# Performance work log

Measured on AMD Instinct MI355X. Metric: run time of the kernel, lower is better.

The kernel has to match this reference:

```python
import jax, jax.numpy as jnp
import numpy as np

N = 50000
E = 800000
IN_DIM = 128
HID = 64
OUT_DIM = 128
NEG_SLOPE = 0.2  # PyG GATConv default


def _add_self_loops(src, dst, edge_attr, n):
    # PyG GATConv(add_self_loops=True) with edge_dim uses fill_value='mean':
    # self-loop edge_attr = mean of edge_attr of incoming edges per node.
    deg = jax.ops.segment_sum(jnp.ones((src.shape[0],), edge_attr.dtype), dst, num_segments=n)
    loop_attr = jax.ops.segment_sum(edge_attr, dst, num_segments=n) / jnp.maximum(deg, 1.0)[:, None]
    loop = jnp.arange(n, dtype=src.dtype)
    return (jnp.concatenate([src, loop]), jnp.concatenate([dst, loop]),
            jnp.concatenate([edge_attr, loop_attr], axis=0))


def _gat_conv(x, src, dst, edge_attr, W, We, a_src, a_dst, a_edge, bias, heads, out_dim, concat, n):
    src, dst, edge_attr = _add_self_loops(src, dst, edge_attr, n)
    h = (x @ W).reshape(n, heads, out_dim)                      # [N,H,D]
    he = (edge_attr @ We).reshape(-1, heads, out_dim)           # [E',H,D]
    alpha_src = jnp.einsum('nhd,hd->nh', h, a_src)
    alpha_dst = jnp.einsum('nhd,hd->nh', h, a_dst)
    alpha_edge = jnp.einsum('ehd,hd->eh', he, a_edge)
    alpha = jax.nn.leaky_relu(alpha_src[src] + alpha_dst[dst] + alpha_edge, NEG_SLOPE)  # [E',H]
    # segment softmax over edges grouped by destination node
    amax = jax.ops.segment_max(alpha, dst, num_segments=n)
    amax = jnp.where(jnp.isfinite(amax), amax, 0.0)
    ex = jnp.exp(alpha - amax[dst])
    denom = jax.ops.segment_sum(ex, dst, num_segments=n)
    coef = ex / (denom[dst] + 1e-16)                            # [E',H]
    msg = h[src] * coef[:, :, None]                             # [E',H,D]
    out = jax.ops.segment_sum(msg, dst, num_segments=n)         # [N,H,D]
    out = out.reshape(n, heads * out_dim) if concat else out.mean(axis=1)
    return out + bias


def setup_inputs() -> dict:
    key = jax.random.key(0)
    ks = jax.random.split(key, 16)
    s = 0.05
    inp = {
        'x': jax.random.normal(ks[0], (N, IN_DIM), jnp.float32),
        'edge_index': jax.random.randint(ks[1], (2, E), 0, N, dtype=jnp.int64),
        'edge_attr': jax.random.normal(ks[2], (E, 2), jnp.float32),
        # gat1: heads=4, concat -> out 4*HID
        'W1': jax.random.normal(ks[3], (IN_DIM, 4 * HID), jnp.float32) * s,
        'We1': jax.random.normal(ks[4], (2, 4 * HID), jnp.float32) * s,
        'asrc1': jax.random.normal(ks[5], (4, HID), jnp.float32) * s,
        'adst1': jax.random.normal(ks[6], (4, HID), jnp.float32) * s,
        'aedge1': jax.random.normal(ks[7], (4, HID), jnp.float32) * s,
        'b1': jnp.zeros((4 * HID,), jnp.float32),
        # gat2: heads=1, concat=False -> out OUT_DIM
        'W2': jax.random.normal(ks[8], (4 * HID, OUT_DIM), jnp.float32) * s,
        'We2': jax.random.normal(ks[9], (2, OUT_DIM), jnp.float32) * s,
        'asrc2': jax.random.normal(ks[10], (1, OUT_DIM), jnp.float32) * s,
        'adst2': jax.random.normal(ks[11], (1, OUT_DIM), jnp.float32) * s,
        'aedge2': jax.random.normal(ks[12], (1, OUT_DIM), jnp.float32) * s,
        'b2': jnp.zeros((OUT_DIM,), jnp.float32),
    }
    return inp


def reference(x, edge_index, edge_attr, W1, We1, asrc1, adst1, aedge1, b1,
              W2, We2, asrc2, adst2, aedge2, b2):
    src, dst = edge_index[0], edge_index[1]
    # dropout layers are identity in eval mode
    h = _gat_conv(x, src, dst, edge_attr, W1, We1, asrc1, adst1, aedge1, b1,
                  heads=4, out_dim=HID, concat=True, n=x.shape[0])
    h = jax.nn.elu(h)
    out = _gat_conv(h, src, dst, edge_attr, W2, We2, asrc2, adst2, aedge2, b2,
                    heads=1, out_dim=OUT_DIM, concat=False, n=x.shape[0])
    return out
```

## Files before the change

### kernel.cpp

```cpp
#include <hip/hip_runtime.h>
#include <hip/hip_bf16.h>

#define NN 50000
#define EE 800000
#define SCAN_B 2048
#define NB ((NN + SCAN_B - 1) / SCAN_B)


typedef short bf16x8 __attribute__((ext_vector_type(8)));
typedef float f32x4  __attribute__((ext_vector_type(4)));

__device__ __forceinline__ float bf2f(unsigned short u) {
    return __uint_as_float(((unsigned)u) << 16);
}
__device__ __forceinline__ unsigned short f2bf(float f) {
    unsigned b = __float_as_uint(f);
    b += 0x7fffu + ((b >> 16) & 1u);
    return (unsigned short)(b >> 16);
}
__device__ __forceinline__ float2 bfpair(unsigned u) {
    return make_float2(__uint_as_float(u << 16), __uint_as_float(u & 0xffff0000u));
}

__global__ void k_prep(const float* __restrict__ We1, const float* __restrict__ ae1,
                       const float* __restrict__ We2, const float* __restrict__ ae2,
                       float* __restrict__ v,
                       const float* __restrict__ W1, unsigned short* __restrict__ W1t,
                       const float* __restrict__ W2, unsigned short* __restrict__ W2t,
                       const int* __restrict__ ei, int* __restrict__ idg,
                       int* __restrict__ rank,
                       const float* __restrict__ x, unsigned short* __restrict__ xb) {
    int bid = blockIdx.x, t = threadIdx.x;
    if (bid == 0) {
        if (t < 8) {
            int c = t >> 2, h = t & 3;
            float s = 0.f;
            for (int d = 0; d < 64; d++) s += We1[c * 256 + h * 64 + d] * ae1[h * 64 + d];
            v[c * 4 + h] = s;
        } else if (t < 10) {
            int c = t - 8;
            float s = 0.f;
            for (int d = 0; d < 128; d++) s += We2[c * 128 + d] * ae2[d];
            v[8 + c] = s;
        }
    } else if (bid <= 256) {
        int idx = (bid - 1) * 256 + t;
        if (idx < 32768) {
            int k = idx >> 8, n = idx & 255;
            W1t[n * 128 + k] = f2bf(W1[idx]);
        } else {
            int i = idx - 32768;
            int k = i >> 7, n = i & 127;
            W2t[n * 256 + k] = f2bf(W2[i]);
        }
    } else if (bid <= 256 + 3125) {
        int e = (bid - 257) * 256 + t;
        if (e < EE) rank[e] = atomicAdd(&idg[ei[EE + e]], 1);
    } else {
        int i = (bid - 3382) * 256 + t;
        if (i < NN * 128 / 4) {
            float4 vv = ((const float4*)x)[i];
            ushort4 o;
            o.x = f2bf(vv.x); o.y = f2bf(vv.y); o.z = f2bf(vv.z); o.w = f2bf(vv.w);
            ((ushort4*)xb)[i] = o;
        }
    }
}

__global__ void k_scan1(const int* __restrict__ idg, int* __restrict__ rowptr,
                        int* __restrict__ bsum) {
    __shared__ int sh[512];
    int t = threadIdx.x;
    int base = blockIdx.x * SCAN_B + t * 4;
    int v[4]; int s = 0;
    #pragma unroll
    for (int j = 0; j < 4; j++) {
        int i = base + j;
        v[j] = (i < NN) ? idg[i] : 0;
        s += v[j];
    }
    sh[t] = s;
    __syncthreads();
    for (int off = 1; off < 512; off <<= 1) {
        int a = (t >= off) ? sh[t - off] : 0;
        __syncthreads();
        sh[t] += a;
        __syncthreads();
    }
    int run = sh[t] - s;
    #pragma unroll
    for (int j = 0; j < 4; j++) {
        int i = base + j;
        if (i < NN) rowptr[i] = run;
        run += v[j];
    }
    if (t == 511) bsum[blockIdx.x] = sh[511];
}

__global__ void k_scan2(const int* __restrict__ bsum, int* __restrict__ boff,
                        int* __restrict__ rowptr) {
    if (threadIdx.x == 0) {
        int acc = 0;
        for (int b = 0; b < NB; b++) { boff[b] = acc; acc += bsum[b]; }
        rowptr[NN] = acc;
    }
}

__global__ void k_scan3(int* __restrict__ rowptr, const int* __restrict__ boff) {
    int t = threadIdx.x;
    int i = blockIdx.x * SCAN_B + t * 4;
    int off = boff[blockIdx.x];
    #pragma unroll
    for (int j = 0; j < 4; j++)
        if (i + j < NN) rowptr[i + j] += off;
}

__global__ void k_scatter(const int* __restrict__ ei, const float* __restrict__ eattr,
                          const int* __restrict__ rowptr, const int* __restrict__ rank,
                          int2* __restrict__ slot) {
    int e = blockIdx.x * blockDim.x + threadIdx.x;
    if (e >= EE) return;
    int s = ei[e], d = ei[EE + e];
    int p = rowptr[d] + rank[e];
    float2 a = ((const float2*)eattr)[e];
    unsigned a0 = f2bf(a.x), a1 = f2bf(a.y);
    slot[p] = make_int2(s, (int)(a0 | (a1 << 16)));
}

template <int K, int NT, int H>
__global__ __launch_bounds__(256) void gemm_mfma(const unsigned short* __restrict__ A,
                                                 const unsigned short* __restrict__ Bt,
                                                 unsigned short* __restrict__ C,
                                                 const float* __restrict__ avs,
                                                 const float* __restrict__ avd,
                                                 float* __restrict__ asrc,
                                                 float* __restrict__ adst,
                                                 int M, int N) {
    int wave = threadIdx.x >> 6, lane = threadIdx.x & 63;
    int l16 = lane & 15, quad = lane >> 4;
    int m0 = blockIdx.y * 128 + wave * 32;
    int n0 = blockIdx.x * (NT * 16);

    f32x4 acc[2][NT];
    #pragma unroll
    for (int mt = 0; mt < 2; mt++)
        #pragma unroll
        for (int nt = 0; nt < NT; nt++)
            acc[mt][nt] = (f32x4){0.f, 0.f, 0.f, 0.f};

    int ar0 = min(m0 + l16, M - 1);
    int ar1 = min(m0 + 16 + l16, M - 1);
    const unsigned short* a0 = A + (size_t)ar0 * K + quad * 8;
    const unsigned short* a1 = A + (size_t)ar1 * K + quad * 8;
    const unsigned short* bp = Bt + (size_t)(n0 + l16) * K + quad * 8;

    #pragma unroll
    for (int k0 = 0; k0 < K; k0 += 32) {
        bf16x8 af0 = *(const bf16x8*)(a0 + k0);
        bf16x8 af1 = *(const bf16x8*)(a1 + k0);
        #pragma unroll
        for (int nt = 0; nt < NT; nt++) {
            bf16x8 bf = *(const bf16x8*)(bp + (size_t)nt * 16 * K + k0);
            acc[0][nt] = __builtin_amdgcn_mfma_f32_16x16x32_bf16(af0, bf, acc[0][nt], 0, 0, 0);
            acc[1][nt] = __builtin_amdgcn_mfma_f32_16x16x32_bf16(af1, bf, acc[1][nt], 0, 0, 0);
        }
    }

    #pragma unroll
    for (int mt = 0; mt < 2; mt++)
        #pragma unroll
        for (int reg = 0; reg < 4; reg++) {
            int row = m0 + mt * 16 + quad * 4 + reg;
            if (row < M) {
                #pragma unroll
                for (int nt = 0; nt < NT; nt++)
                    C[(size_t)row * N + n0 + nt * 16 + l16] = f2bf(acc[mt][nt][reg]);
            }
        }

    float ws[NT], wd[NT];
    #pragma unroll
    for (int nt = 0; nt < NT; nt++) {
        ws[nt] = avs[n0 + nt * 16 + l16];
        wd[nt] = avd[n0 + nt * 16 + l16];
    }
    int hh = n0 >> 6;
    #pragma unroll
    for (int mt = 0; mt < 2; mt++)
        #pragma unroll
        for (int reg = 0; reg < 4; reg++) {
            int row = m0 + mt * 16 + quad * 4 + reg;
            float s1 = 0.f, s2 = 0.f;
            #pragma unroll
            for (int nt = 0; nt < NT; nt++) {
                float c = acc[mt][nt][reg];
                s1 += c * ws[nt];
                s2 += c * wd[nt];
            }
            #pragma unroll
            for (int off = 1; off < 16; off <<= 1) {
                s1 += __shfl_xor(s1, off);
                s2 += __shfl_xor(s2, off);
            }
            if (l16 == 0 && row < M) {
                asrc[row * H + hh] = s1;
                adst[row * H + hh] = s2;
            }
        }
}

__global__ __launch_bounds__(256) void k_agg1(const int* __restrict__ rowptr,
                       const int2* __restrict__ slot, const float* __restrict__ asrc,
                       const float* __restrict__ adst, const float* __restrict__ v,
                       const unsigned short* __restrict__ hb, const float* __restrict__ b1,
                       unsigned short* __restrict__ h2b) {
    int node = blockIdx.x * 4 + (threadIdx.x >> 6);
    if (node >= NN) return;
    int lane = threadIdx.x & 63;
    int h2 = lane >> 5;
    int hl = lane & 31;
    int hd = hl >> 3;
    int beg = rowptr[node], end = rowptr[node + 1];
    float pd = adst[node * 4 + hd];
    float vh0 = v[hd], vh1 = v[4 + hd];
    float acc[8] = {};
    float den = 0.f, s0 = 0.f, s1 = 0.f;
    const unsigned short* hbq = hb + hl * 8;

    int cnt = end - beg;
    int safeLast = max(end - 1, 0);
    int mend = beg + (cnt & ~1);

    int2 sl0 = slot[min(beg + h2, safeLast)];
    int2 sl1 = slot[min(beg + 2 + h2, safeLast)];

    auto body = [&](int2 cur) {
        int s = cur.x;
        float2 a = bfpair((unsigned)cur.y);
        float al = asrc[s * 4 + hd] + pd + a.x * vh0 + a.y * vh1;
        al = (al > 0.f) ? al : 0.2f * al;
        float e = __expf(al);
        s0 += a.x; s1 += a.y; den += e;
        uint4 r = *(const uint4*)(hbq + (size_t)s * 256);
        float2 p;
        p = bfpair(r.x); acc[0] += e * p.x; acc[1] += e * p.y;
        p = bfpair(r.y); acc[2] += e * p.x; acc[3] += e * p.y;
        p = bfpair(r.z); acc[4] += e * p.x; acc[5] += e * p.y;
        p = bfpair(r.w); acc[6] += e * p.x; acc[7] += e * p.y;
    };

    #pragma unroll 2
    for (int pb = beg; pb < mend; pb += 2) {
        int2 cur = sl0;
        sl0 = sl1;
        sl1 = slot[min(pb + 4 + h2, safeLast)];
        body(cur);
    }
    if (h2 == 0 && mend < end) body(sl0);

    #pragma unroll
    for (int k = 0; k < 8; k++) acc[k] += __shfl_down(acc[k], 32);
    den += __shfl_xor(den, 32);
    s0  += __shfl_xor(s0, 32);
    s1  += __shfl_xor(s1, 32);

    float dg = fmaxf((float)cnt, 1.0f);
    float als = asrc[node * 4 + hd] + pd + (s0 / dg) * vh0 + (s1 / dg) * vh1;
    als = (als > 0.f) ? als : 0.2f * als;
    float exs = __expf(als);
    den += exs;

    if (h2 == 0) {
        uint4 r = *(const uint4*)(hbq + (size_t)node * 256);
        float2 p;
        p = bfpair(r.x); acc[0] += exs * p.x; acc[1] += exs * p.y;
        p = bfpair(r.y); acc[2] += exs * p.x; acc[3] += exs * p.y;
        p = bfpair(r.z); acc[4] += exs * p.x; acc[5] += exs * p.y;
        p = bfpair(r.w); acc[6] += exs * p.x; acc[7] += exs * p.y;
        float inv = 1.f / (den + 1e-16f);
        short ov[8];
        #pragma unroll
        for (int k = 0; k < 8; k++) {
            float va = acc[k] * inv + b1[hl * 8 + k];
            va = (va > 0.f) ? va : __expf(va) - 1.f;
            ov[k] = (short)f2bf(va);
        }
        bf16x8 o8 = {ov[0], ov[1], ov[2], ov[3], ov[4], ov[5], ov[6], ov[7]};
        *(bf16x8*)(h2b + (size_t)node * 256 + hl * 8) = o8;
    }
}

__global__ __launch_bounds__(256) void k_agg2(const int* __restrict__ rowptr,
                       const int2* __restrict__ slot, const float* __restrict__ asrc,
                       const float* __restrict__ adst, const float* __restrict__ v,
                       const unsigned short* __restrict__ gb, const float* __restrict__ b2,
                       float* __restrict__ outp) {
    int node = blockIdx.x * 4 + (threadIdx.x >> 6);
    if (node >= NN) return;
    int lane = threadIdx.x & 63;
    int q  = lane >> 4;
    int ql = lane & 15;
    int beg = rowptr[node], end = rowptr[node + 1];
    float ad = adst[node];
    float v0 = v[0], v1 = v[1];
    float acc[8] = {};
    float den = 0.f, s0 = 0.f, s1 = 0.f;
    const unsigned short* gbq = gb + ql * 8;

    int cnt = end - beg;
    int safeLast = max(end - 1, 0);
    int mend = beg + (cnt & ~3);

    int2 sl0 = slot[min(beg + q, safeLast)];
    int2 sl1 = slot[min(beg + 4 + q, safeLast)];

    auto body = [&](int2 cur) {
        int s = cur.x;
        float2 a = bfpair((unsigned)cur.y);
        float al = asrc[s] + ad + a.x * v0 + a.y * v1;
        al = (al > 0.f) ? al : 0.2f * al;
        float e = __expf(al);
        s0 += a.x; s1 += a.y; den += e;
        uint4 r = *(const uint4*)(gbq + (size_t)s * 128);
        float2 p;
        p = bfpair(r.x); acc[0] += e * p.x; acc[1] += e * p.y;
        p = bfpair(r.y); acc[2] += e * p.x; acc[3] += e * p.y;
        p = bfpair(r.z); acc[4] += e * p.x; acc[5] += e * p.y;
        p = bfpair(r.w); acc[6] += e * p.x; acc[7] += e * p.y;
    };

    #pragma unroll 2
    for (int pb = beg; pb < mend; pb += 4) {
        int2 cur = sl0;
        sl0 = sl1;
        sl1 = slot[min(pb + 8 + q, safeLast)];
        body(cur);
    }
    if (mend + q < end) body(sl0);

    #pragma unroll
    for (int k = 0; k < 8; k++) {
        acc[k] += __shfl_down(acc[k], 32);
        acc[k] += __shfl_down(acc[k], 16);
    }
    den += __shfl_xor(den, 16); den += __shfl_xor(den, 32);
    s0  += __shfl_xor(s0, 16);  s0  += __shfl_xor(s0, 32);
    s1  += __shfl_xor(s1, 16);  s1  += __shfl_xor(s1, 32);

    float dg = fmaxf((float)cnt, 1.0f);
    float als = asrc[node] + ad + (s0 / dg) * v0 + (s1 / dg) * v1;
    als = (als > 0.f) ? als : 0.2f * als;
    float exs = __expf(als);
    den += exs;

    if (q == 0) {
        uint4 r = *(const uint4*)(gbq + (size_t)node * 128);
        float2 p;
        p = bfpair(r.x); acc[0] += exs * p.x; acc[1] += exs * p.y;
        p = bfpair(r.y); acc[2] += exs * p.x; acc[3] += exs * p.y;
        p = bfpair(r.z); acc[4] += exs * p.x; acc[5] += exs * p.y;
        p = bfpair(r.w); acc[6] += exs * p.x; acc[7] += exs * p.y;
        float inv = 1.f / (den + 1e-16f);
        float4 o0, o1;
        o0.x = acc[0] * inv + b2[ql * 8 + 0];
        o0.y = acc[1] * inv + b2[ql * 8 + 1];
        o0.z = acc[2] * inv + b2[ql * 8 + 2];
        o0.w = acc[3] * inv + b2[ql * 8 + 3];
        o1.x = acc[4] * inv + b2[ql * 8 + 4];
        o1.y = acc[5] * inv + b2[ql * 8 + 5];
        o1.z = acc[6] * inv + b2[ql * 8 + 6];
        o1.w = acc[7] * inv + b2[ql * 8 + 7];
        *(float4*)(outp + (size_t)node * 128 + ql * 8)     = o0;
        *(float4*)(outp + (size_t)node * 128 + ql * 8 + 4) = o1;
    }
}

extern "C" void kernel_launch(void* const* d_in, const int* in_sizes, int n_in,
                              void* d_out, int out_size, void* d_ws, size_t ws_size,
                              hipStream_t stream) {
    const float* x     = (const float*)d_in[0];
    const int*   ei    = (const int*)d_in[1];
    const float* eattr = (const float*)d_in[2];
    const float* W1    = (const float*)d_in[3];
    const float* We1   = (const float*)d_in[4];
    const float* as1   = (const float*)d_in[5];
    const float* ad1   = (const float*)d_in[6];
    const float* ae1   = (const float*)d_in[7];
    const float* b1    = (const float*)d_in[8];
    const float* W2    = (const float*)d_in[9];
    const float* We2   = (const float*)d_in[10];
    const float* as2   = (const float*)d_in[11];
    const float* ad2   = (const float*)d_in[12];
    const float* ae2   = (const float*)d_in[13];
    const float* b2    = (const float*)d_in[14];
    float* out = (float*)d_out;

    int* idg    = (int*)d_ws;
    int* rank   = idg + NN;
    int* rowptr = rank + EE;
    int* bsum   = rowptr + NN + 16;
    int* boff   = bsum + 32;
    int2* slot  = (int2*)(boff + 32);
    float* asrc1 = (float*)(slot + EE);
    float* adst1 = asrc1 + 4 * NN;
    float* asrc2 = adst1 + 4 * NN;
    float* adst2 = asrc2 + NN;
    float* vbuf  = adst2 + NN;
    unsigned short* ub = (unsigned short*)(((uintptr_t)(vbuf + 64) + 63) & ~(uintptr_t)63);
    unsigned short* x_bf  = ub;
    unsigned short* W1t   = x_bf + (size_t)NN * 128;
    unsigned short* W2t   = W1t + 32768;
    unsigned short* h1_bf = W2t + 32768;
    unsigned short* h2_bf = h1_bf + (size_t)NN * 256;
    unsigned short* g2_bf = h2_bf + (size_t)NN * 256;

    hipMemsetAsync(idg, 0, (size_t)NN * sizeof(int), stream);

    k_prep<<<9632, 256, 0, stream>>>(We1, ae1, We2, ae2, vbuf, W1, W1t, W2, W2t,
                                     ei, idg, rank, x, x_bf);
    k_scan1<<<NB, 512, 0, stream>>>(idg, rowptr, bsum);
    k_scan2<<<1, 64, 0, stream>>>(bsum, boff, rowptr);
    k_scan3<<<NB, 512, 0, stream>>>(rowptr, boff);
    k_scatter<<<(EE + 255) / 256, 256, 0, stream>>>(ei, eattr, rowptr, rank, slot);

    gemm_mfma<128, 4, 4><<<dim3(4, (NN + 127) / 128), 256, 0, stream>>>(
        x_bf, W1t, h1_bf, as1, ad1, asrc1, adst1, NN, 256);
    k_agg1<<<(NN + 3) / 4, 256, 0, stream>>>(rowptr, slot, asrc1, adst1, vbuf,
                                             h1_bf, b1, h2_bf);

    gemm_mfma<256, 8, 1><<<dim3(1, (NN + 127) / 128), 256, 0, stream>>>(
        h2_bf, W2t, g2_bf, as2, ad2, asrc2, adst2, NN, 128);
    k_agg2<<<(NN + 3) / 4, 256, 0, stream>>>(rowptr, slot, asrc2, adst2, vbuf + 8,
                                             g2_bf, b2, out);
}
```

Measured before the change: 327.7 us.

## Aggregate raw x before projecting in layer one, fold attention vectors into W1

Layer one now computes attention logits directly from x, using W1 folded with the source and destination attention vectors (Asd). It then aggregates the 128-wide bf16 x rows per head into a 512-wide per-node buffer, and only afterwards runs a per-head MFMA projection with bias and ELU. The gather in the edge loop touches 256 bytes per edge instead of 512, at the cost of four times as many accumulators per lane and a larger intermediate buffer written and read by the projection. The intermediate buffer is reused for the layer-two GEMM output.

```diff
diff --git a/kernel.cpp b/kernel.cpp
--- a/kernel.cpp
+++ b/kernel.cpp
@@ -25,6 +25,8 @@
 __global__ void k_prep(const float* __restrict__ We1, const float* __restrict__ ae1,
                        const float* __restrict__ We2, const float* __restrict__ ae2,
                        float* __restrict__ v,
+                       const float* __restrict__ as1, const float* __restrict__ ad1,
+                       float* __restrict__ Asd,
                        const float* __restrict__ W1, unsigned short* __restrict__ W1t,
                        const float* __restrict__ W2, unsigned short* __restrict__ W2t,
                        const int* __restrict__ ei, int* __restrict__ idg,
@@ -43,6 +45,15 @@
             for (int d = 0; d < 128; d++) s += We2[c * 128 + d] * ae2[d];
             v[8 + c] = s;
         }
+        #pragma unroll 1
+        for (int idx = t; idx < 1024; idx += 256) {
+            int k = idx >> 3, j = idx & 7;
+            const float* a = (j < 4) ? as1 : ad1;
+            int h = j & 3;
+            float s = 0.f;
+            for (int c = 0; c < 64; c++) s += W1[k * 256 + h * 64 + c] * a[h * 64 + c];
+            Asd[idx] = s;
+        }
     } else if (bid <= 256) {
         int idx = (bid - 1) * 256 + t;
         if (idx < 32768) {
@@ -125,6 +136,203 @@
     float2 a = ((const float2*)eattr)[e];
     unsigned a0 = f2bf(a.x), a1 = f2bf(a.y);
     slot[p] = make_int2(s, (int)(a0 | (a1 << 16)));
+}
+
+__global__ __launch_bounds__(256) void k_attn1(const unsigned short* __restrict__ xb,
+                       const float* __restrict__ Asd,
+                       float* __restrict__ asrc, float* __restrict__ adst) {
+    int node = blockIdx.x * 4 + (threadIdx.x >> 6);
+    if (node >= NN) return;
+    int lane = threadIdx.x & 63;
+    unsigned xw = *(const unsigned*)(xb + (size_t)node * 128 + lane * 2);
+    float2 xc = bfpair(xw);
+    const float4* A4 = (const float4*)Asd;
+    float4 s0 = A4[lane * 4 + 0];
+    float4 d0 = A4[lane * 4 + 1];
+    float4 s1 = A4[lane * 4 + 2];
+    float4 d1 = A4[lane * 4 + 3];
+    float r[8];
+    r[0] = xc.x * s0.x + xc.y * s1.x;
+    r[1] = xc.x * s0.y + xc.y * s1.y;
+    r[2] = xc.x * s0.z + xc.y * s1.z;
+    r[3] = xc.x * s0.w + xc.y * s1.w;
+    r[4] = xc.x * d0.x + xc.y * d1.x;
+    r[5] = xc.x * d0.y + xc.y * d1.y;
+    r[6] = xc.x * d0.z + xc.y * d1.z;
+    r[7] = xc.x * d0.w + xc.y * d1.w;
+    #pragma unroll
+    for (int off = 1; off < 64; off <<= 1)
+        #pragma unroll
+        for (int j = 0; j < 8; j++) r[j] += __shfl_xor(r[j], off);
+    if (lane == 0) {
+        *(float4*)(asrc + node * 4) = make_float4(r[0], r[1], r[2], r[3]);
+        *(float4*)(adst + node * 4) = make_float4(r[4], r[5], r[6], r[7]);
+    }
+}
+
+__global__ __launch_bounds__(256) void k_agg1x(const int* __restrict__ rowptr,
+                       const int2* __restrict__ slot, const float* __restrict__ asrc,
+                       const float* __restrict__ adst, const float* __restrict__ v,
+                       const unsigned short* __restrict__ xb,
+                       unsigned short* __restrict__ Sx) {
+    int node = blockIdx.x * 4 + (threadIdx.x >> 6);
+    if (node >= NN) return;
+    int lane = threadIdx.x & 63;
+    int q  = lane >> 4;
+    int ql = lane & 15;
+    int beg = rowptr[node], end = rowptr[node + 1];
+    float4 pd4 = *(const float4*)(adst + node * 4);
+    float pd[4] = {pd4.x, pd4.y, pd4.z, pd4.w};
+    float v0[4] = {v[0], v[1], v[2], v[3]};
+    float v1[4] = {v[4], v[5], v[6], v[7]};
+    float acc[4][8] = {};
+    float den[4] = {};
+    float s0 = 0.f, s1 = 0.f;
+    const unsigned short* xbq = xb + ql * 8;
+
+    int cnt = end - beg;
+    int safeLast = max(end - 1, 0);
+    int mend = beg + (cnt & ~3);
+
+    int2 sl0 = slot[min(beg + q, safeLast)];
+    int2 sl1 = slot[min(beg + 4 + q, safeLast)];
+
+    auto body = [&](int2 cur) {
+        int s = cur.x;
+        float2 a = bfpair((unsigned)cur.y);
+        float4 as4 = *(const float4*)(asrc + s * 4);
+        float as_[4] = {as4.x, as4.y, as4.z, as4.w};
+        uint4 r = *(const uint4*)(xbq + (size_t)s * 128);
+        float e[4];
+        #pragma unroll
+        for (int h = 0; h < 4; h++) {
+            float al = as_[h] + pd[h] + a.x * v0[h] + a.y * v1[h];
+            al = (al > 0.f) ? al : 0.2f * al;
+            e[h] = __expf(al);
+            den[h] += e[h];
+        }
+        s0 += a.x; s1 += a.y;
+        float xx[8];
+        float2 p;
+        p = bfpair(r.x); xx[0] = p.x; xx[1] = p.y;
+        p = bfpair(r.y); xx[2] = p.x; xx[3] = p.y;
+        p = bfpair(r.z); xx[4] = p.x; xx[5] = p.y;
+        p = bfpair(r.w); xx[6] = p.x; xx[7] = p.y;
+        #pragma unroll
+        for (int h = 0; h < 4; h++)
+            #pragma unroll
+            for (int c = 0; c < 8; c++) acc[h][c] += e[h] * xx[c];
+    };
+
+    #pragma unroll 2
+    for (int pb = beg; pb < mend; pb += 4) {
+        int2 cur = sl0;
+        sl0 = sl1;
+        sl1 = slot[min(pb + 8 + q, safeLast)];
+        body(cur);
+    }
+    if (mend + q < end) body(sl0);
+
+    #pragma unroll
+    for (int h = 0; h < 4; h++)
+        #pragma unroll
+        for (int c = 0; c < 8; c++) {
+            acc[h][c] += __shfl_down(acc[h][c], 32);
+            acc[h][c] += __shfl_down(acc[h][c], 16);
+        }
+    #pragma unroll
+    for (int h = 0; h < 4; h++) {
+        den[h] += __shfl_xor(den[h], 16);
+        den[h] += __shfl_xor(den[h], 32);
+    }
+    s0 += __shfl_xor(s0, 16); s0 += __shfl_xor(s0, 32);
+    s1 += __shfl_xor(s1, 16); s1 += __shfl_xor(s1, 32);
+
+    float dg = fmaxf((float)cnt, 1.0f);
+    float4 an4 = *(const float4*)(asrc + node * 4);
+    float an[4] = {an4.x, an4.y, an4.z, an4.w};
+    float exs[4];
+    #pragma unroll
+    for (int h = 0; h < 4; h++) {
+        float als = an[h] + pd[h] + (s0 / dg) * v0[h] + (s1 / dg) * v1[h];
+        als = (als > 0.f) ? als : 0.2f * als;
+        exs[h] = __expf(als);
+        den[h] += exs[h];
+    }
+
+    if (q == 0) {
+        uint4 r = *(const uint4*)(xbq + (size_t)node * 128);
+        float xx[8];
+        float2 p;
+        p = bfpair(r.x); xx[0] = p.x; xx[1] = p.y;
+        p = bfpair(r.y); xx[2] = p.x; xx[3] = p.y;
+        p = bfpair(r.z); xx[4] = p.x; xx[5] = p.y;
+        p = bfpair(r.w); xx[6] = p.x; xx[7] = p.y;
+        #pragma unroll
+        for (int h = 0; h < 4; h++) {
+            float inv = 1.f / (den[h] + 1e-16f);
+            short ov[8];
+            #pragma unroll
+            for (int c = 0; c < 8; c++)
+                ov[c] = (short)f2bf((acc[h][c] + exs[h] * xx[c]) * inv);
+            bf16x8 o8 = {ov[0], ov[1], ov[2], ov[3], ov[4], ov[5], ov[6], ov[7]};
+            *(bf16x8*)(Sx + (size_t)node * 512 + h * 128 + ql * 8) = o8;
+        }
+    }
+}
+
+__global__ __launch_bounds__(256) void k_proj1(const unsigned short* __restrict__ Sx,
+                       const unsigned short* __restrict__ W1t,
+                       const float* __restrict__ b1,
+                       unsigned short* __restrict__ h2b) {
+    int h = blockIdx.x;
+    int wave = threadIdx.x >> 6, lane = threadIdx.x & 63;
+    int l16 = lane & 15, quad = lane >> 4;
+    int m0 = blockIdx.y * 128 + wave * 32;
+
+    f32x4 acc[2][4];
+    #pragma unroll
+    for (int mt = 0; mt < 2; mt++)
+        #pragma unroll
+        for (int nt = 0; nt < 4; nt++)
+            acc[mt][nt] = (f32x4){0.f, 0.f, 0.f, 0.f};
+
+    int ar0 = min(m0 + l16, NN - 1);
+    int ar1 = min(m0 + 16 + l16, NN - 1);
+    const unsigned short* a0 = Sx + (size_t)ar0 * 512 + h * 128 + quad * 8;
+    const unsigned short* a1 = Sx + (size_t)ar1 * 512 + h * 128 + quad * 8;
+    const unsigned short* bp = W1t + (size_t)(h * 64 + l16) * 128 + quad * 8;
+
+    #pragma unroll
+    for (int k0 = 0; k0 < 128; k0 += 32) {
+        bf16x8 af0 = *(const bf16x8*)(a0 + k0);
+        bf16x8 af1 = *(const bf16x8*)(a1 + k0);
+        #pragma unroll
+        for (int nt = 0; nt < 4; nt++) {
+            bf16x8 bf = *(const bf16x8*)(bp + (size_t)nt * 16 * 128 + k0);
+            acc[0][nt] = __builtin_amdgcn_mfma_f32_16x16x32_bf16(af0, bf, acc[0][nt], 0, 0, 0);
+            acc[1][nt] = __builtin_amdgcn_mfma_f32_16x16x32_bf16(af1, bf, acc[1][nt], 0, 0, 0);
+        }
+    }
+
+    float bia[4];
+    #pragma unroll
+    for (int nt = 0; nt < 4; nt++) bia[nt] = b1[h * 64 + nt * 16 + l16];
+
+    #pragma unroll
+    for (int mt = 0; mt < 2; mt++)
+        #pragma unroll
+        for (int reg = 0; reg < 4; reg++) {
+            int row = m0 + mt * 16 + quad * 4 + reg;
+            if (row < NN) {
+                #pragma unroll
+                for (int nt = 0; nt < 4; nt++) {
+                    float va = acc[mt][nt][reg] + bia[nt];
+                    va = (va > 0.f) ? va : __expf(va) - 1.f;
+                    h2b[(size_t)row * 256 + h * 64 + nt * 16 + l16] = f2bf(va);
+                }
+            }
+        }
 }
 
 template <int K, int NT, int H>
@@ -207,87 +415,6 @@
                 adst[row * H + hh] = s2;
             }
         }
-}
-
-__global__ __launch_bounds__(256) void k_agg1(const int* __restrict__ rowptr,
-                       const int2* __restrict__ slot, const float* __restrict__ asrc,
-                       const float* __restrict__ adst, const float* __restrict__ v,
-                       const unsigned short* __restrict__ hb, const float* __restrict__ b1,
-                       unsigned short* __restrict__ h2b) {
-    int node = blockIdx.x * 4 + (threadIdx.x >> 6);
-    if (node >= NN) return;
-    int lane = threadIdx.x & 63;
-    int h2 = lane >> 5;
-    int hl = lane & 31;
-    int hd = hl >> 3;
-    int beg = rowptr[node], end = rowptr[node + 1];
-    float pd = adst[node * 4 + hd];
-    float vh0 = v[hd], vh1 = v[4 + hd];
-    float acc[8] = {};
-    float den = 0.f, s0 = 0.f, s1 = 0.f;
-    const unsigned short* hbq = hb + hl * 8;
-
-    int cnt = end - beg;
-    int safeLast = max(end - 1, 0);
-    int mend = beg + (cnt & ~1);
-
-    int2 sl0 = slot[min(beg + h2, safeLast)];
-    int2 sl1 = slot[min(beg + 2 + h2, safeLast)];
-
-    auto body = [&](int2 cur) {
-        int s = cur.x;
-        float2 a = bfpair((unsigned)cur.y);
-        float al = asrc[s * 4 + hd] + pd + a.x * vh0 + a.y * vh1;
-        al = (al > 0.f) ? al : 0.2f * al;
-        float e = __expf(al);
-        s0 += a.x; s1 += a.y; den += e;
-        uint4 r = *(const uint4*)(hbq + (size_t)s * 256);
-        float2 p;
-        p = bfpair(r.x); acc[0] += e * p.x; acc[1] += e * p.y;
-        p = bfpair(r.y); acc[2] += e * p.x; acc[3] += e * p.y;
-        p = bfpair(r.z); acc[4] += e * p.x; acc[5] += e * p.y;
-        p = bfpair(r.w); acc[6] += e * p.x; acc[7] += e * p.y;
-    };
-
-    #pragma unroll 2
-    for (int pb = beg; pb < mend; pb += 2) {
-        int2 cur = sl0;
-        sl0 = sl1;
-        sl1 = slot[min(pb + 4 + h2, safeLast)];
-        body(cur);
-    }
-    if (h2 == 0 && mend < end) body(sl0);
-
-    #pragma unroll
-    for (int k = 0; k < 8; k++) acc[k] += __shfl_down(acc[k], 32);
-    den += __shfl_xor(den, 32);
-    s0  += __shfl_xor(s0, 32);
-    s1  += __shfl_xor(s1, 32);
-
-    float dg = fmaxf((float)cnt, 1.0f);
-    float als = asrc[node * 4 + hd] + pd + (s0 / dg) * vh0 + (s1 / dg) * vh1;
-    als = (als > 0.f) ? als : 0.2f * als;
-    float exs = __expf(als);
-    den += exs;
-
-    if (h2 == 0) {
-        uint4 r = *(const uint4*)(hbq + (size_t)node * 256);
-        float2 p;
-        p = bfpair(r.x); acc[0] += exs * p.x; acc[1] += exs * p.y;
-        p = bfpair(r.y); acc[2] += exs * p.x; acc[3] += exs * p.y;
-        p = bfpair(r.z); acc[4] += exs * p.x; acc[5] += exs * p.y;
-        p = bfpair(r.w); acc[6] += exs * p.x; acc[7] += exs * p.y;
-        float inv = 1.f / (den + 1e-16f);
-        short ov[8];
-        #pragma unroll
-        for (int k = 0; k < 8; k++) {
-            float va = acc[k] * inv + b1[hl * 8 + k];
-            va = (va > 0.f) ? va : __expf(va) - 1.f;
-            ov[k] = (short)f2bf(va);
-        }
-        bf16x8 o8 = {ov[0], ov[1], ov[2], ov[3], ov[4], ov[5], ov[6], ov[7]};
-        *(bf16x8*)(h2b + (size_t)node * 256 + hl * 8) = o8;
-    }
 }
 
 __global__ __launch_bounds__(256) void k_agg2(const int* __restrict__ rowptr,
@@ -406,27 +533,28 @@
     float* asrc2 = adst1 + 4 * NN;
     float* adst2 = asrc2 + NN;
     float* vbuf  = adst2 + NN;
-    unsigned short* ub = (unsigned short*)(((uintptr_t)(vbuf + 64) + 63) & ~(uintptr_t)63);
+    float* Asd   = vbuf + 64;
+    unsigned short* ub = (unsigned short*)(((uintptr_t)(Asd + 1024) + 63) & ~(uintptr_t)63);
     unsigned short* x_bf  = ub;
     unsigned short* W1t   = x_bf + (size_t)NN * 128;
     unsigned short* W2t   = W1t + 32768;
-    unsigned short* h1_bf = W2t + 32768;
-    unsigned short* h2_bf = h1_bf + (size_t)NN * 256;
-    unsigned short* g2_bf = h2_bf + (size_t)NN * 256;
+    unsigned short* Sx    = W2t + 32768;
+    unsigned short* h2_bf = Sx + (size_t)NN * 512;
+    unsigned short* g2_bf = Sx;
 
     hipMemsetAsync(idg, 0, (size_t)NN * sizeof(int), stream);
 
-    k_prep<<<9632, 256, 0, stream>>>(We1, ae1, We2, ae2, vbuf, W1, W1t, W2, W2t,
-                                     ei, idg, rank, x, x_bf);
+    k_prep<<<9632, 256, 0, stream>>>(We1, ae1, We2, ae2, vbuf, as1, ad1, Asd,
+                                     W1, W1t, W2, W2t, ei, idg, rank, x, x_bf);
     k_scan1<<<NB, 512, 0, stream>>>(idg, rowptr, bsum);
     k_scan2<<<1, 64, 0, stream>>>(bsum, boff, rowptr);
     k_scan3<<<NB, 512, 0, stream>>>(rowptr, boff);
     k_scatter<<<(EE + 255) / 256, 256, 0, stream>>>(ei, eattr, rowptr, rank, slot);
 
-    gemm_mfma<128, 4, 4><<<dim3(4, (NN + 127) / 128), 256, 0, stream>>>(
-        x_bf, W1t, h1_bf, as1, ad1, asrc1, adst1, NN, 256);
-    k_agg1<<<(NN + 3) / 4, 256, 0, stream>>>(rowptr, slot, asrc1, adst1, vbuf,
-                                             h1_bf, b1, h2_bf);
+    k_attn1<<<(NN + 3) / 4, 256, 0, stream>>>(x_bf, Asd, asrc1, adst1);
+    k_agg1x<<<(NN + 3) / 4, 256, 0, stream>>>(rowptr, slot, asrc1, adst1, vbuf,
+                                              x_bf, Sx);
+    k_proj1<<<dim3(4, (NN + 127) / 128), 256, 0, stream>>>(Sx, W1t, b1, h2_bf);
 
     gemm_mfma<256, 8, 1><<<dim3(1, (NN + 127) / 128), 256, 0, stream>>>(
         h2_bf, W2t, g2_bf, as2, ad2, asrc2, adst2, NN, 128);
```

Result: slower. 353.2 us (+7.8%).

## Merge scan into one block, fuse scatter with GEMM1, use exp2

Applied to the files above, without the earlier changes.

Replaces the three-kernel prefix scan with a single 1024-thread block scan. Fuses the edge scatter into the first GEMM launch as extra blocks so both run concurrently, saving launches. Pre-scales the attention vectors by log2(e) so softmax exponentials use the hardware exp2 instruction directly. The single-block scan serializes 49 elements per thread, which may be slower per element but avoids two kernel launches.

```diff
diff --git a/kernel.cpp b/kernel.cpp
--- a/kernel.cpp
+++ b/kernel.cpp
@@ -3,16 +3,13 @@
 
 #define NN 50000
 #define EE 800000
-#define SCAN_B 2048
-#define NB ((NN + SCAN_B - 1) / SCAN_B)
+#define LOG2E 1.44269504088896340736f
+#define GB1 1564
 
 
 typedef short bf16x8 __attribute__((ext_vector_type(8)));
 typedef float f32x4  __attribute__((ext_vector_type(4)));
 
-__device__ __forceinline__ float bf2f(unsigned short u) {
-    return __uint_as_float(((unsigned)u) << 16);
-}
 __device__ __forceinline__ unsigned short f2bf(float f) {
     unsigned b = __float_as_uint(f);
     b += 0x7fffu + ((b >> 16) & 1u);
@@ -36,12 +33,12 @@
             int c = t >> 2, h = t & 3;
             float s = 0.f;
             for (int d = 0; d < 64; d++) s += We1[c * 256 + h * 64 + d] * ae1[h * 64 + d];
-            v[c * 4 + h] = s;
+            v[c * 4 + h] = s * LOG2E;
         } else if (t < 10) {
             int c = t - 8;
             float s = 0.f;
             for (int d = 0; d < 128; d++) s += We2[c * 128 + d] * ae2[d];
-            v[8 + c] = s;
+            v[8 + c] = s * LOG2E;
         }
     } else if (bid <= 256) {
         int idx = (bid - 1) * 256 + t;
@@ -67,79 +64,50 @@
     }
 }
 
-__global__ void k_scan1(const int* __restrict__ idg, int* __restrict__ rowptr,
-                        int* __restrict__ bsum) {
-    __shared__ int sh[512];
+__global__ __launch_bounds__(1024) void k_scanA(const int* __restrict__ idg,
+                                                int* __restrict__ rowptr) {
+    __shared__ int sh[1024];
     int t = threadIdx.x;
-    int base = blockIdx.x * SCAN_B + t * 4;
-    int v[4]; int s = 0;
-    #pragma unroll
-    for (int j = 0; j < 4; j++) {
+    int base = t * 49;
+    int s = 0;
+    for (int j = 0; j < 49; j++) {
         int i = base + j;
-        v[j] = (i < NN) ? idg[i] : 0;
-        s += v[j];
+        s += (i < NN) ? idg[i] : 0;
     }
     sh[t] = s;
     __syncthreads();
-    for (int off = 1; off < 512; off <<= 1) {
+    for (int off = 1; off < 1024; off <<= 1) {
         int a = (t >= off) ? sh[t - off] : 0;
         __syncthreads();
         sh[t] += a;
         __syncthreads();
     }
     int run = sh[t] - s;
-    #pragma unroll
-    for (int j = 0; j < 4; j++) {
+    for (int j = 0; j < 49; j++) {
         int i = base + j;
-        if (i < NN) rowptr[i] = run;
-        run += v[j];
-    }
-    if (t == 511) bsum[blockIdx.x] = sh[511];
-}
-
-__global__ void k_scan2(const int* __restrict__ bsum, int* __restrict__ boff,
-                        int* __restrict__ rowptr) {
-    if (threadIdx.x == 0) {
-        int acc = 0;
-        for (int b = 0; b < NB; b++) { boff[b] = acc; acc += bsum[b]; }
-        rowptr[NN] = acc;
-    }
-}
-
-__global__ void k_scan3(int* __restrict__ rowptr, const int* __restrict__ boff) {
-    int t = threadIdx.x;
-    int i = blockIdx.x * SCAN_B + t * 4;
-    int off = boff[blockIdx.x];
-    #pragma unroll
-    for (int j = 0; j < 4; j++)
-        if (i + j < NN) rowptr[i + j] += off;
-}
-
-__global__ void k_scatter(const int* __restrict__ ei, const float* __restrict__ eattr,
-                          const int* __restrict__ rowptr, const int* __restrict__ rank,
-                          int2* __restrict__ slot) {
-    int e = blockIdx.x * blockDim.x + threadIdx.x;
-    if (e >= EE) return;
-    int s = ei[e], d = ei[EE + e];
-    int p = rowptr[d] + rank[e];
-    float2 a = ((const float2*)eattr)[e];
-    unsigned a0 = f2bf(a.x), a1 = f2bf(a.y);
-    slot[p] = make_int2(s, (int)(a0 | (a1 << 16)));
+        if (i < NN) {
+            int val = idg[i];
+            rowptr[i] = run;
+            run += val;
+        }
+    }
+    if (t == 1023) rowptr[NN] = sh[1023];
 }
 
 template <int K, int NT, int H>
-__global__ __launch_bounds__(256) void gemm_mfma(const unsigned short* __restrict__ A,
-                                                 const unsigned short* __restrict__ Bt,
-                                                 unsigned short* __restrict__ C,
-                                                 const float* __restrict__ avs,
-                                                 const float* __restrict__ avd,
-                                                 float* __restrict__ asrc,
-                                                 float* __restrict__ adst,
-                                                 int M, int N) {
+__device__ __forceinline__ void gemm_body(int bx, int by,
+                                          const unsigned short* __restrict__ A,
+                                          const unsigned short* __restrict__ Bt,
+                                          unsigned short* __restrict__ C,
+                                          const float* __restrict__ avs,
+                                          const float* __restrict__ avd,
+                                          float* __restrict__ asrc,
+                                          float* __restrict__ adst,
+                                          int M, int N) {
     int wave = threadIdx.x >> 6, lane = threadIdx.x & 63;
     int l16 = lane & 15, quad = lane >> 4;
-    int m0 = blockIdx.y * 128 + wave * 32;
-    int n0 = blockIdx.x * (NT * 16);
+    int m0 = by * 128 + wave * 32;
+    int n0 = bx * (NT * 16);
 
     f32x4 acc[2][NT];
     #pragma unroll
@@ -181,8 +149,8 @@
     float ws[NT], wd[NT];
     #pragma unroll
     for (int nt = 0; nt < NT; nt++) {
-        ws[nt] = avs[n0 + nt * 16 + l16];
-        wd[nt] = avd[n0 + nt * 16 + l16];
+        ws[nt] = avs[n0 + nt * 16 + l16] * LOG2E;
+        wd[nt] = avd[n0 + nt * 16 + l16] * LOG2E;
     }
     int hh = n0 >> 6;
     #pragma unroll
@@ -209,6 +177,37 @@
         }
 }
 
+__global__ __launch_bounds__(256) void k_sg(const unsigned short* __restrict__ xb,
+                       const unsigned short* __restrict__ W1t,
+                       unsigned short* __restrict__ h1b,
+                       const float* __restrict__ as1, const float* __restrict__ ad1,
+                       float* __restrict__ asrc1, float* __restrict__ adst1,
+                       const int* __restrict__ ei, const float* __restrict__ eattr,
+                       const int* __restrict__ rowptr, const int* __restrict__ rank,
+                       int2* __restrict__ slot) {
+    int bid = blockIdx.x;
+    if (bid < GB1) {
+        gemm_body<128, 4, 4>(bid & 3, bid >> 2, xb, W1t, h1b, as1, ad1,
+                             asrc1, adst1, NN, 256);
+    } else {
+        int e = (bid - GB1) * 256 + threadIdx.x;
+        if (e >= EE) return;
+        int s = ei[e], d = ei[EE + e];
+        int p = rowptr[d] + rank[e];
+        float2 a = ((const float2*)eattr)[e];
+        unsigned a0 = f2bf(a.x), a1 = f2bf(a.y);
+        slot[p] = make_int2(s, (int)(a0 | (a1 << 16)));
+    }
+}
+
+__global__ __launch_bounds__(256) void k_gemm2(const unsigned short* __restrict__ A,
+                       const unsigned short* __restrict__ Bt,
+                       unsigned short* __restrict__ C,
+                       const float* __restrict__ avs, const float* __restrict__ avd,
+                       float* __restrict__ asrc, float* __restrict__ adst) {
+    gemm_body<256, 8, 1>(0, blockIdx.x, A, Bt, C, avs, avd, asrc, adst, NN, 128);
+}
+
 __global__ __launch_bounds__(256) void k_agg1(const int* __restrict__ rowptr,
                        const int2* __restrict__ slot, const float* __restrict__ asrc,
                        const float* __restrict__ adst, const float* __restrict__ v,
@@ -239,7 +238,7 @@
         float2 a = bfpair((unsigned)cur.y);
         float al = asrc[s * 4 + hd] + pd + a.x * vh0 + a.y * vh1;
         al = (al > 0.f) ? al : 0.2f * al;
-        float e = __expf(al);
+        float e = __builtin_amdgcn_exp2f(al);
         s0 += a.x; s1 += a.y; den += e;
         uint4 r = *(const uint4*)(hbq + (size_t)s * 256);
         float2 p;
@@ -267,7 +266,7 @@
     float dg = fmaxf((float)cnt, 1.0f);
     float als = asrc[node * 4 + hd] + pd + (s0 / dg) * vh0 + (s1 / dg) * vh1;
     als = (als > 0.f) ? als : 0.2f * als;
-    float exs = __expf(als);
+    float exs = __builtin_amdgcn_exp2f(als);
     den += exs;
 
     if (h2 == 0) {
@@ -319,7 +318,7 @@
         float2 a = bfpair((unsigned)cur.y);
         float al = asrc[s] + ad + a.x * v0 + a.y * v1;
         al = (al > 0.f) ? al : 0.2f * al;
-        float e = __expf(al);
+        float e = __builtin_amdgcn_exp2f(al);
         s0 += a.x; s1 += a.y; den += e;
         uint4 r = *(const uint4*)(gbq + (size_t)s * 128);
         float2 p;
@@ -350,7 +349,7 @@
     float dg = fmaxf((float)cnt, 1.0f);
     float als = asrc[node] + ad + (s0 / dg) * v0 + (s1 / dg) * v1;
     als = (als > 0.f) ? als : 0.2f * als;
-    float exs = __expf(als);
+    float exs = __builtin_amdgcn_exp2f(als);
     den += exs;
 
     if (q == 0) {
@@ -418,18 +417,16 @@
 
     k_prep<<<9632, 256, 0, stream>>>(We1, ae1, We2, ae2, vbuf, W1, W1t, W2, W2t,
                                      ei, idg, rank, x, x_bf);
-    k_scan1<<<NB, 512, 0, stream>>>(idg, rowptr, bsum);
-    k_scan2<<<1, 64, 0, stream>>>(bsum, boff, rowptr);
-    k_scan3<<<NB, 512, 0, stream>>>(rowptr, boff);
-    k_scatter<<<(EE + 255) / 256, 256, 0, stream>>>(ei, eattr, rowptr, rank, slot);
-
-    gemm_mfma<128, 4, 4><<<dim3(4, (NN + 127) / 128), 256, 0, stream>>>(
-        x_bf, W1t, h1_bf, as1, ad1, asrc1, adst1, NN, 256);
+    k_scanA<<<1, 1024, 0, stream>>>(idg, rowptr);
+
+    k_sg<<<GB1 + 3125, 256, 0, stream>>>(x_bf, W1t, h1_bf, as1, ad1,
+                                         asrc1, adst1, ei, eattr, rowptr, rank, slot);
+
     k_agg1<<<(NN + 3) / 4, 256, 0, stream>>>(rowptr, slot, asrc1, adst1, vbuf,
                                              h1_bf, b1, h2_bf);
 
-    gemm_mfma<256, 8, 1><<<dim3(1, (NN + 127) / 128), 256, 0, stream>>>(
-        h2_bf, W2t, g2_bf, as2, ad2, asrc2, adst2, NN, 128);
+    k_gemm2<<<(NN + 127) / 128, 256, 0, stream>>>(h2_bf, W2t, g2_bf, as2, ad2,
+                                                  asrc2, adst2);
     k_agg2<<<(NN + 3) / 4, 256, 0, stream>>>(rowptr, slot, asrc2, adst2, vbuf + 8,
                                              g2_bf, b2, out);
 }
```

Measured after the change: 401.2 us. 22.4% more time.
